# Kernel tuning notes

Hardware: AMD Instinct MI355X
Metric: run time of the kernel (lower is better)

The kernel has to match this reference:

```python
import jax, jax.numpy as jnp
import numpy as np

B, S, D = 4, 2048, 1024
H, DK, DV = 16, 64, 64
TEMP = (4 * DK) ** 0.5
EPS = 1e-6


def setup_inputs() -> dict:
    key = jax.random.key(0)
    ks = jax.random.split(key, 16)
    def lin(k, fin, fout):
        # torch Linear default init: U(-1/sqrt(fin), 1/sqrt(fin)); weight stored [fout,fin], we use [fin,fout]
        bound = 1.0 / np.sqrt(fin)
        return jax.random.uniform(k, (fin, fout), jnp.float32, -bound, bound)
    inp = {}
    for i, name in enumerate(['q_a', 'k_a', 'v_a', 'q_s', 'k_s', 'v_s']):
        inp[name] = jax.random.normal(ks[i], (B, S, D), jnp.float32)
    inp['Wqa'] = lin(ks[6], D, H * DK)
    inp['Wka'] = lin(ks[7], D, H * DK)
    inp['Wva'] = lin(ks[8], D, H * DV)
    inp['Wqs'] = lin(ks[9], D, H * DK)
    inp['Wks'] = lin(ks[10], D, H * DK)
    inp['Wvs'] = lin(ks[11], D, H * DV)
    inp['Wfc'] = lin(ks[12], H * DV, D)
    inp['gamma'] = jnp.ones((D,), jnp.float32)
    inp['beta'] = jnp.zeros((D,), jnp.float32)
    return inp


def _proj(x, W, dh):
    # [B,S,D] @ [D,H*dh] -> [B,H,S,dh]
    b, s, _ = x.shape
    return (x @ W).reshape(b, s, H, dh).transpose(0, 2, 1, 3)


def reference(q_a, k_a, v_a, q_s, k_s, v_s, Wqa, Wka, Wva, Wqs, Wks, Wvs, Wfc, gamma, beta):
    residual = q_a + q_s
    qa = _proj(q_a, Wqa, DK)
    ka = _proj(k_a, Wka, DK)
    va = _proj(v_a, Wva, DV)
    qs = _proj(q_s, Wqs, DK)
    ks = _proj(k_s, Wks, DK)
    vs = _proj(v_s, Wvs, DV)
    # a2a + a2s + s2a + s2s == (qa+qs) @ (ka+ks)^T  (same math, single GEMM)
    scores = jnp.einsum('bhqd,bhkd->bhqk', qa + qs, ka + ks) / TEMP
    attn = jax.nn.softmax(scores, axis=-1)  # [B,H,S,S]
    ctx = jnp.einsum('bhqk,bhkd->bhqd', attn, va + vs)
    ctx = ctx.transpose(0, 2, 1, 3).reshape(q_a.shape[0], q_a.shape[1], H * DV)
    out = ctx @ Wfc + residual
    mu = jnp.mean(out, axis=-1, keepdims=True)
    var = jnp.var(out, axis=-1, keepdims=True)
    out = (out - mu) * jax.lax.rsqrt(var + EPS) * gamma + beta
    return out
```

## Files before the change

### kernel.cpp

```cpp
#include <hip/hip_runtime.h>
#include <hip/hip_bf16.h>
#include <cstdint>
#include <cstddef>

typedef __bf16 bf16;
typedef __bf16 bf16x8 __attribute__((ext_vector_type(8)));
typedef __bf16 bf16x4v __attribute__((ext_vector_type(4)));
typedef __bf16 bf16x2v __attribute__((ext_vector_type(2)));
typedef float f32x4 __attribute__((ext_vector_type(4)));
typedef float f32x16 __attribute__((ext_vector_type(16)));
typedef unsigned uint2v __attribute__((ext_vector_type(2)));
typedef unsigned uint4v __attribute__((ext_vector_type(4)));

#define MFMA16(a, b, c) __builtin_amdgcn_mfma_f32_16x16x32_bf16((a), (b), (c), 0, 0, 0)
#define MFMA32(a, b, c) __builtin_amdgcn_mfma_f32_32x32x16_bf16((a), (b), (c), 0, 0, 0)
#define SWZ(row, byte) ((((row) * 128) + (byte)) ^ (((row) & 7) << 4))

constexpr int BB = 4, SS = 2048, DD = 1024, HH = 16;
constexpr int NROWS = BB * SS;
constexpr size_t NB = (size_t)NROWS * DD;
constexpr size_t NW = (size_t)DD * DD;

static __device__ __forceinline__ unsigned pk2(float a, float b) {
    bf16x2v h;
    h[0] = (bf16)a; h[1] = (bf16)b;
    return __builtin_bit_cast(unsigned, h);
}

static __device__ __forceinline__ bf16x8 frag4(unsigned w0, unsigned w1, unsigned w2, unsigned w3) {
    uint4v u;
    u[0] = w0; u[1] = w1; u[2] = w2; u[3] = w3;
    return __builtin_bit_cast(bf16x8, u);
}

struct Ptrs6 { const float* p[6]; };

__global__ __launch_bounds__(256) void cvt_in_kernel(Ptrs6 src, bf16* dst) {
    const int z = blockIdx.y;
    const size_t idx = (size_t)blockIdx.x * 256 + threadIdx.x;
    float4 v = ((const float4*)src.p[z])[idx];
    bf16x4v o;
    o[0] = (bf16)v.x; o[1] = (bf16)v.y; o[2] = (bf16)v.z; o[3] = (bf16)v.w;
    *(bf16x4v*)(dst + z * NB + idx * 4) = o;
}

struct Ptrs7 { const float* p[7]; };

__global__ __launch_bounds__(256) void cvt_w_kernel(Ptrs7 src, bf16* dst) {
    const int z = blockIdx.z;
    const float* W = src.p[z];
    bf16* WT = dst + (size_t)z * NW;
    __shared__ float tile[32][33];
    const int tx = threadIdx.x, ty = threadIdx.y;
    const int kb = blockIdx.y * 32, nb = blockIdx.x * 32;
#pragma unroll
    for (int j = 0; j < 4; ++j)
        tile[ty + j * 8][tx] = W[(size_t)(kb + ty + j * 8) * DD + nb + tx];
    __syncthreads();
#pragma unroll
    for (int j = 0; j < 4; ++j)
        WT[(size_t)(nb + ty + j * 8) * DD + kb + tx] = (bf16)tile[tx][ty + j * 8];
}

__global__ __launch_bounds__(256) void vt_kernel(const bf16* __restrict__ V,
                                                 bf16* __restrict__ Vt) {
    const int bh = blockIdx.y;
    const int s0 = blockIdx.x * 64;
    __shared__ bf16 t[64][72];
    const int tid = threadIdx.x;
    const int row = tid >> 2, seg = tid & 3;
    const bf16* src = V + ((size_t)bh * SS + s0 + row) * 64 + seg * 16;
    bf16x8 v0 = *(const bf16x8*)src;
    bf16x8 v1 = *(const bf16x8*)(src + 8);
#pragma unroll
    for (int j = 0; j < 8; ++j) {
        t[seg * 16 + j][row] = v0[j];
        t[seg * 16 + 8 + j][row] = v1[j];
    }
    __syncthreads();
    const int d = tid >> 2, c = (tid & 3) * 16;
    bf16x8 o0 = *(const bf16x8*)(&t[d][c]);
    bf16x8 o1 = *(const bf16x8*)(&t[d][c + 8]);
    bf16* dst = Vt + ((size_t)bh * 64 + d) * SS + s0 + c;
    *(bf16x8*)dst = o0;
    *(bf16x8*)(dst + 8) = o1;
}

struct GemmPtrs {
    const bf16* a1[3]; const bf16* a2[3];
    const bf16* b1[3]; const bf16* b2[3];
    bf16* outbh[3];
};

template <int MODE>
__global__ __launch_bounds__(256) void gemm_kernel(GemmPtrs P, int iters, int split,
                                                   float* outF, const float* r1, const float* r2) {
    const int z = blockIdx.z;
    const bf16* __restrict__ A1 = P.a1[z];
    const bf16* __restrict__ A2 = P.a2[z];
    const bf16* __restrict__ B1 = P.b1[z];
    const bf16* __restrict__ B2 = P.b2[z];

    const int tid = threadIdx.x;
    const int lane = tid & 63, w = tid >> 6;
    const int g = lane >> 4, i = lane & 15;
    const int m0 = blockIdx.y * 128, n0 = blockIdx.x * 128;
    const int mb = (w >> 1) * 64, nb = (w & 1) * 64;

    __shared__ __align__(16) bf16 As[128 * 64];
    __shared__ __align__(16) bf16 Bs[128 * 64];

    f32x4 acc[4][4];
#pragma unroll
    for (int a = 0; a < 4; ++a)
#pragma unroll
        for (int b = 0; b < 4; ++b) acc[a][b] = 0.0f;

    for (int kt = 0; kt < iters; ++kt) {
        const bf16* Ag; const bf16* Bg; int koff;
        if (kt < split) { Ag = A1; Bg = B1; koff = kt * 64; }
        else            { Ag = A2; Bg = B2; koff = (kt - split) * 64; }

        __syncthreads();
#pragma unroll
        for (int c = 0; c < 4; ++c) {
            int ci = c * 256 + tid;
            int row = ci >> 3, seg = ci & 7;
            int lb = (row * 128 + seg * 16) ^ ((row & 7) << 4);
            const bf16* ap;
            if (MODE == 0) {
                ap = Ag + (size_t)(m0 + row) * DD + koff + seg * 8;
            } else {
                int gr = m0 + row;
                ap = Ag + ((size_t)((gr >> 11) * HH + (koff >> 6)) * SS + (gr & 2047)) * 64 + seg * 8;
            }
            bf16x8 va = *(const bf16x8*)ap;
            bf16x8 vb = *(const bf16x8*)(Bg + (size_t)(n0 + row) * DD + koff + seg * 8);
            *(bf16x8*)((char*)As + lb) = va;
            *(bf16x8*)((char*)Bs + lb) = vb;
        }
        __syncthreads();

#pragma unroll
        for (int f = 0; f < 2; ++f) {
            bf16x8 af[4], bff[4];
#pragma unroll
            for (int mt = 0; mt < 4; ++mt) {
                int row = mb + mt * 16 + i;
                af[mt] = *(const bf16x8*)((char*)As + ((row * 128 + f * 64 + g * 16) ^ ((row & 7) << 4)));
            }
#pragma unroll
            for (int nt = 0; nt < 4; ++nt) {
                int row = nb + nt * 16 + i;
                bff[nt] = *(const bf16x8*)((char*)Bs + ((row * 128 + f * 64 + g * 16) ^ ((row & 7) << 4)));
            }
#pragma unroll
            for (int mt = 0; mt < 4; ++mt)
#pragma unroll
                for (int nt = 0; nt < 4; ++nt)
                    acc[mt][nt] = MFMA16(af[mt], bff[nt], acc[mt][nt]);
        }
    }

    if (MODE == 0) {
        bf16* outQ = P.outbh[z];
#pragma unroll
        for (int mt = 0; mt < 4; ++mt)
#pragma unroll
            for (int nt = 0; nt < 4; ++nt) {
                int colg = n0 + nb + nt * 16 + i;
                int h = colg >> 6, d = colg & 63;
#pragma unroll
                for (int r = 0; r < 4; ++r) {
                    int rowg = m0 + mb + mt * 16 + g * 4 + r;
                    int b = rowg >> 11, s = rowg & 2047;
                    outQ[(((size_t)(b * HH + h)) * SS + s) * 64 + d] = (bf16)acc[mt][nt][r];
                }
            }
    } else {
#pragma unroll
        for (int mt = 0; mt < 4; ++mt)
#pragma unroll
            for (int nt = 0; nt < 4; ++nt) {
                int colg = n0 + nb + nt * 16 + i;
#pragma unroll
                for (int r = 0; r < 4; ++r) {
                    int rowg = m0 + mb + mt * 16 + g * 4 + r;
                    size_t off = (size_t)rowg * DD + colg;
                    outF[off] = acc[mt][nt][r] + r1[off] + r2[off];
                }
            }
    }
}

__global__ __launch_bounds__(512, 4) void attn_kernel(const bf16* __restrict__ Qg,
                                                      const bf16* __restrict__ Kg,
                                                      const bf16* __restrict__ Vt,
                                                      bf16* __restrict__ ctxh) {
    const int bid = blockIdx.x;
    const int bh = ((bid & 7) << 3) | (bid >> 6);
    const int qt = (bid >> 3) & 7;

    const int tid = threadIdx.x;
    const int lane = tid & 63, w = tid >> 6;
    const int hi = lane >> 5, q = lane & 31;

    __shared__ __align__(16) char smem[32768];

    const int qrow = qt * 256 + w * 32 + q;
    bf16x8 qf[4];
    {
        const bf16* qp = Qg + ((size_t)bh * SS + qrow) * 64;
#pragma unroll
        for (int c = 0; c < 4; ++c) {
            bf16x8 v = *(const bf16x8*)(qp + c * 16 + hi * 8);
#pragma unroll
            for (int e = 0; e < 8; ++e) v[e] = (bf16)((float)v[e] * 0.0625f);
            qf[c] = v;
        }
    }

    const int srow = tid >> 3, sseg = tid & 7;
    const bf16* kgp = Kg + (size_t)bh * SS * 64;
    const bf16* vgp = Vt + (size_t)bh * 64 * SS;
    const int sbyte = SWZ(srow, sseg * 16);

    bf16x8 kreg = *(const bf16x8*)(kgp + (size_t)srow * 64 + sseg * 8);
    bf16x8 vreg = *(const bf16x8*)(vgp + (size_t)srow * SS + sseg * 8);

    f32x16 o0 = {}, o1 = {};
    float m = -3e38f, l = 0.0f;

    for (int kt = 0; kt < SS / 64; ++kt) {
        char* kb_ = smem + (kt & 1) * 16384;
        char* vb_ = kb_ + 8192;
        *(bf16x8*)(kb_ + sbyte) = kreg;
        *(bf16x8*)(vb_ + sbyte) = vreg;
        if (kt + 1 < SS / 64) {
            const int k0n = (kt + 1) * 64;
            kreg = *(const bf16x8*)(kgp + (size_t)(k0n + srow) * 64 + sseg * 8);
            vreg = *(const bf16x8*)(vgp + (size_t)srow * SS + k0n + sseg * 8);
        }
        __syncthreads();

        f32x16 st0 = {}, st1 = {};
#pragma unroll
        for (int c = 0; c < 4; ++c) {
            bf16x8 kf = *(const bf16x8*)(kb_ + SWZ(q, c * 32 + hi * 16));
            st0 = MFMA32(kf, qf[c], st0);
        }
#pragma unroll
        for (int c = 0; c < 4; ++c) {
            bf16x8 kf = *(const bf16x8*)(kb_ + SWZ(32 + q, c * 32 + hi * 16));
            st1 = MFMA32(kf, qf[c], st1);
        }

        float tm = st0[0];
#pragma unroll
        for (int r = 1; r < 16; ++r) tm = fmaxf(tm, st0[r]);
#pragma unroll
        for (int r = 0; r < 16; ++r) tm = fmaxf(tm, st1[r]);
        tm = fmaxf(tm, __shfl_xor(tm, 32, 64));
        if (!__all(tm - m <= 8.0f)) {
            float nm = fmaxf(m, tm);
            float al = __expf(m - nm);
            l *= al;
            o0 *= al;
            o1 *= al;
            m = nm;
        }
        float sum = 0.0f;
#pragma unroll
        for (int r = 0; r < 16; ++r) { st0[r] = __expf(st0[r] - m); sum += st0[r]; }
#pragma unroll
        for (int r = 0; r < 16; ++r) { st1[r] = __expf(st1[r] - m); sum += st1[r]; }
        l += sum;

        bf16x8 pf[4];
#pragma unroll
        for (int c = 0; c < 4; ++c) {
            const f32x16 s_ = (c < 2) ? st0 : st1;
            const int b0 = (c & 1) * 8;
            unsigned a0 = pk2(s_[b0 + 0], s_[b0 + 1]);
            unsigned c0 = pk2(s_[b0 + 4], s_[b0 + 5]);
            unsigned a1 = pk2(s_[b0 + 2], s_[b0 + 3]);
            unsigned c1 = pk2(s_[b0 + 6], s_[b0 + 7]);
            uint2v s1 = __builtin_amdgcn_permlane32_swap(a0, c0, false, false);
            uint2v s2 = __builtin_amdgcn_permlane32_swap(a1, c1, false, false);
            pf[c] = frag4(s1[0], s2[0], s1[1], s2[1]);
        }

#pragma unroll
        for (int c = 0; c < 4; ++c) {
            bf16x8 vf = *(const bf16x8*)(vb_ + SWZ(q, c * 32 + hi * 16));
            o0 = MFMA32(vf, pf[c], o0);
        }
#pragma unroll
        for (int c = 0; c < 4; ++c) {
            bf16x8 vf = *(const bf16x8*)(vb_ + SWZ(32 + q, c * 32 + hi * 16));
            o1 = MFMA32(vf, pf[c], o1);
        }
    }

    float lt = l + __shfl_xor(l, 32, 64);
    float rl = 1.0f / lt;
    __syncthreads();
    const int orow = w * 32 + q;
#pragma unroll
    for (int dh = 0; dh < 2; ++dh) {
#pragma unroll
        for (int r = 0; r < 16; r += 2) {
            float v0 = (dh ? o1[r] : o0[r]) * rl;
            float v1 = (dh ? o1[r + 1] : o0[r + 1]) * rl;
            int d = dh * 32 + (r & 3) + 8 * (r >> 2) + 4 * hi;
            *(unsigned*)(smem + SWZ(orow, d * 2)) = pk2(v0, v1);
        }
    }
    __syncthreads();
    {
        const int row = tid >> 1, hf = tid & 1;
        bf16* outp = ctxh + ((size_t)bh * SS + qt * 256 + row) * 64 + hf * 32;
#pragma unroll
        for (int c = 0; c < 4; ++c) {
            bf16x8 v = *(const bf16x8*)(smem + SWZ(row, hf * 64 + c * 16));
            *(bf16x8*)(outp + c * 8) = v;
        }
    }
}

__global__ __launch_bounds__(256) void ln_kernel(const float* __restrict__ tmp,
                                                 const float* __restrict__ gamma,
                                                 const float* __restrict__ beta,
                                                 float* __restrict__ out) {
    const int row = blockIdx.x;
    const int t = threadIdx.x;
    float4 v = ((const float4*)(tmp + (size_t)row * DD))[t];
    float s = v.x + v.y + v.z + v.w;
    float ss = v.x * v.x + v.y * v.y + v.z * v.z + v.w * v.w;
#pragma unroll
    for (int mask = 1; mask <= 32; mask <<= 1) {
        s += __shfl_xor(s, mask, 64);
        ss += __shfl_xor(ss, mask, 64);
    }
    __shared__ float red[8];
    const int w = t >> 6, lane = t & 63;
    if (lane == 0) { red[w] = s; red[4 + w] = ss; }
    __syncthreads();
    s = red[0] + red[1] + red[2] + red[3];
    ss = red[4] + red[5] + red[6] + red[7];
    const float mu = s * (1.0f / 1024.0f);
    const float var = ss * (1.0f / 1024.0f) - mu * mu;
    const float rs = rsqrtf(var + 1e-6f);
    float4 gm = ((const float4*)gamma)[t];
    float4 bt = ((const float4*)beta)[t];
    float4 ov;
    ov.x = (v.x - mu) * rs * gm.x + bt.x;
    ov.y = (v.y - mu) * rs * gm.y + bt.y;
    ov.z = (v.z - mu) * rs * gm.z + bt.z;
    ov.w = (v.w - mu) * rs * gm.w + bt.w;
    ((float4*)(out + (size_t)row * DD))[t] = ov;
}

extern "C" void kernel_launch(void* const* d_in, const int* in_sizes, int n_in,
                              void* d_out, int out_size, void* d_ws, size_t ws_size,
                              hipStream_t stream) {
    (void)in_sizes; (void)n_in; (void)out_size; (void)ws_size;

    char* ws = (char*)d_ws;
    bf16* xb = (bf16*)ws;
    bf16* wT = (bf16*)(ws + 100663296ull);
    bf16* Qg = (bf16*)(ws + 115343360ull);
    bf16* Kg = (bf16*)(ws + 132120576ull);
    bf16* Vg = (bf16*)(ws + 148897792ull);
    bf16* ctxh = (bf16*)ws;
    bf16* Vtg = (bf16*)(ws + 16777216ull);
    float* tmp = (float*)(ws + 33554432ull);

    {
        Ptrs6 p;
        for (int j = 0; j < 6; ++j) p.p[j] = (const float*)d_in[j];
        cvt_in_kernel<<<dim3(8192, 6), 256, 0, stream>>>(p, xb);
    }
    {
        Ptrs7 p;
        for (int j = 0; j < 7; ++j) p.p[j] = (const float*)d_in[6 + j];
        cvt_w_kernel<<<dim3(32, 32, 7), dim3(32, 8), 0, stream>>>(p, wT);
    }
    {
        GemmPtrs gp;
        gp.a1[0] = xb;           gp.a1[1] = xb + NB;     gp.a1[2] = xb + 2 * NB;
        gp.a2[0] = xb + 3 * NB;  gp.a2[1] = xb + 4 * NB; gp.a2[2] = xb + 5 * NB;
        gp.b1[0] = wT;           gp.b1[1] = wT + NW;     gp.b1[2] = wT + 2 * NW;
        gp.b2[0] = wT + 3 * NW;  gp.b2[1] = wT + 4 * NW; gp.b2[2] = wT + 5 * NW;
        gp.outbh[0] = Qg; gp.outbh[1] = Kg; gp.outbh[2] = Vg;
        gemm_kernel<0><<<dim3(8, 64, 3), 256, 0, stream>>>(gp, 32, 16, nullptr, nullptr, nullptr);
    }
    vt_kernel<<<dim3(32, 64), 256, 0, stream>>>(Vg, Vtg);
    attn_kernel<<<dim3(512), 512, 0, stream>>>(Qg, Kg, Vtg, ctxh);
    {
        GemmPtrs gp;
        for (int j = 0; j < 3; ++j) {
            gp.a1[j] = ctxh; gp.a2[j] = ctxh;
            gp.b1[j] = wT + 6 * NW; gp.b2[j] = wT + 6 * NW;
            gp.outbh[j] = nullptr;
        }
        gemm_kernel<1><<<dim3(8, 64, 1), 256, 0, stream>>>(gp, 16, 16, tmp,
                                                           (const float*)d_in[0],
                                                           (const float*)d_in[3]);
    }
    ln_kernel<<<dim3(8192), 256, 0, stream>>>(tmp, (const float*)d_in[13],
                                              (const float*)d_in[14], (float*)d_out);
}
```

Measured before the change: 552.1 us.

## Use direct global-to-LDS loads, XCD-aware block remap, and MFMA priority hints

```diff
diff --git a/kernel.cpp b/kernel.cpp
--- a/kernel.cpp
+++ b/kernel.cpp
@@ -15,6 +15,9 @@
 #define MFMA16(a, b, c) __builtin_amdgcn_mfma_f32_16x16x32_bf16((a), (b), (c), 0, 0, 0)
 #define MFMA32(a, b, c) __builtin_amdgcn_mfma_f32_32x32x16_bf16((a), (b), (c), 0, 0, 0)
 #define SWZ(row, byte) ((((row) * 128) + (byte)) ^ (((row) & 7) << 4))
+#define GLOAD_LDS(g, l) \
+    __builtin_amdgcn_global_load_lds((const __attribute__((address_space(1))) void*)(g), \
+                                     (__attribute__((address_space(3))) void*)(l), 16, 0, 0)
 
 constexpr int BB = 4, SS = 2048, DD = 1024, HH = 16;
 constexpr int NROWS = BB * SS;
@@ -95,7 +98,13 @@
 template <int MODE>
 __global__ __launch_bounds__(256) void gemm_kernel(GemmPtrs P, int iters, int split,
                                                    float* outF, const float* r1, const float* r2) {
-    const int z = blockIdx.z;
+    const int cpx = gridDim.x >> 3;
+    const int bid0 = blockIdx.x;
+    const int work = (bid0 & 7) * cpx + (bid0 >> 3);
+    const int z = work >> 9;
+    const int rem = work & 511;
+    const int m0 = (rem >> 3) * 128, n0 = (rem & 7) * 128;
+
     const bf16* __restrict__ A1 = P.a1[z];
     const bf16* __restrict__ A2 = P.a2[z];
     const bf16* __restrict__ B1 = P.b1[z];
@@ -104,17 +113,19 @@
     const int tid = threadIdx.x;
     const int lane = tid & 63, w = tid >> 6;
     const int g = lane >> 4, i = lane & 15;
-    const int m0 = blockIdx.y * 128, n0 = blockIdx.x * 128;
     const int mb = (w >> 1) * 64, nb = (w & 1) * 64;
 
     __shared__ __align__(16) bf16 As[128 * 64];
     __shared__ __align__(16) bf16 Bs[128 * 64];
 
+    const int lrow = lane >> 3, lseg = lane & 7;
+    const int chunk = lseg ^ lrow;
+
     f32x4 acc[4][4];
 #pragma unroll
-    for (int a = 0; a < 4; ++a)
-#pragma unroll
-        for (int b = 0; b < 4; ++b) acc[a][b] = 0.0f;
+    for (int aa = 0; aa < 4; ++aa)
+#pragma unroll
+        for (int bb = 0; bb < 4; ++bb) acc[aa][bb] = 0.0f;
 
     for (int kt = 0; kt < iters; ++kt) {
         const bf16* Ag; const bf16* Bg; int koff;
@@ -124,20 +135,17 @@
         __syncthreads();
 #pragma unroll
         for (int c = 0; c < 4; ++c) {
-            int ci = c * 256 + tid;
-            int row = ci >> 3, seg = ci & 7;
-            int lb = (row * 128 + seg * 16) ^ ((row & 7) << 4);
+            const int row = (w * 4 + c) * 8 + lrow;
             const bf16* ap;
             if (MODE == 0) {
-                ap = Ag + (size_t)(m0 + row) * DD + koff + seg * 8;
+                ap = Ag + (size_t)(m0 + row) * DD + koff + chunk * 8;
             } else {
                 int gr = m0 + row;
-                ap = Ag + ((size_t)((gr >> 11) * HH + (koff >> 6)) * SS + (gr & 2047)) * 64 + seg * 8;
+                ap = Ag + ((size_t)((gr >> 11) * HH + (koff >> 6)) * SS + (gr & 2047)) * 64 + chunk * 8;
             }
-            bf16x8 va = *(const bf16x8*)ap;
-            bf16x8 vb = *(const bf16x8*)(Bg + (size_t)(n0 + row) * DD + koff + seg * 8);
-            *(bf16x8*)((char*)As + lb) = va;
-            *(bf16x8*)((char*)Bs + lb) = vb;
+            const bf16* bp = Bg + (size_t)(n0 + row) * DD + koff + chunk * 8;
+            GLOAD_LDS(ap, As + (w * 4 + c) * 512);
+            GLOAD_LDS(bp, Bs + (w * 4 + c) * 512);
         }
         __syncthreads();
 
@@ -147,12 +155,12 @@
 #pragma unroll
             for (int mt = 0; mt < 4; ++mt) {
                 int row = mb + mt * 16 + i;
-                af[mt] = *(const bf16x8*)((char*)As + ((row * 128 + f * 64 + g * 16) ^ ((row & 7) << 4)));
+                af[mt] = *(const bf16x8*)((char*)As + SWZ(row, f * 64 + g * 16));
             }
 #pragma unroll
             for (int nt = 0; nt < 4; ++nt) {
                 int row = nb + nt * 16 + i;
-                bff[nt] = *(const bf16x8*)((char*)Bs + ((row * 128 + f * 64 + g * 16) ^ ((row & 7) << 4)));
+                bff[nt] = *(const bf16x8*)((char*)Bs + SWZ(row, f * 64 + g * 16));
             }
 #pragma unroll
             for (int mt = 0; mt < 4; ++mt)
@@ -244,6 +252,7 @@
         __syncthreads();
 
         f32x16 st0 = {}, st1 = {};
+        __builtin_amdgcn_s_setprio(1);
 #pragma unroll
         for (int c = 0; c < 4; ++c) {
             bf16x8 kf = *(const bf16x8*)(kb_ + SWZ(q, c * 32 + hi * 16));
@@ -254,6 +263,7 @@
             bf16x8 kf = *(const bf16x8*)(kb_ + SWZ(32 + q, c * 32 + hi * 16));
             st1 = MFMA32(kf, qf[c], st1);
         }
+        __builtin_amdgcn_s_setprio(0);
 
         float tm = st0[0];
 #pragma unroll
@@ -290,6 +300,7 @@
             pf[c] = frag4(s1[0], s2[0], s1[1], s2[1]);
         }
 
+        __builtin_amdgcn_s_setprio(1);
 #pragma unroll
         for (int c = 0; c < 4; ++c) {
             bf16x8 vf = *(const bf16x8*)(vb_ + SWZ(q, c * 32 + hi * 16));
@@ -300,6 +311,7 @@
             bf16x8 vf = *(const bf16x8*)(vb_ + SWZ(32 + q, c * 32 + hi * 16));
             o1 = MFMA32(vf, pf[c], o1);
         }
+        __builtin_amdgcn_s_setprio(0);
     }
 
     float lt = l + __shfl_xor(l, 32, 64);
@@ -393,7 +405,7 @@
         gp.b1[0] = wT;           gp.b1[1] = wT + NW;     gp.b1[2] = wT + 2 * NW;
         gp.b2[0] = wT + 3 * NW;  gp.b2[1] = wT + 4 * NW; gp.b2[2] = wT + 5 * NW;
         gp.outbh[0] = Qg; gp.outbh[1] = Kg; gp.outbh[2] = Vg;
-        gemm_kernel<0><<<dim3(8, 64, 3), 256, 0, stream>>>(gp, 32, 16, nullptr, nullptr, nullptr);
+        gemm_kernel<0><<<dim3(1536), 256, 0, stream>>>(gp, 32, 16, nullptr, nullptr, nullptr);
     }
     vt_kernel<<<dim3(32, 64), 256, 0, stream>>>(Vg, Vtg);
     attn_kernel<<<dim3(512), 512, 0, stream>>>(Qg, Kg, Vtg, ctxh);
@@ -404,9 +416,9 @@
             gp.b1[j] = wT + 6 * NW; gp.b2[j] = wT + 6 * NW;
             gp.outbh[j] = nullptr;
         }
-        gemm_kernel<1><<<dim3(8, 64, 1), 256, 0, stream>>>(gp, 16, 16, tmp,
-                                                           (const float*)d_in[0],
-                                                           (const float*)d_in[3]);
+        gemm_kernel<1><<<dim3(512), 256, 0, stream>>>(gp, 16, 16, tmp,
+                                                      (const float*)d_in[0],
+                                                      (const float*)d_in[3]);
     }
     ln_kernel<<<dim3(8192), 256, 0, stream>>>(tmp, (const float*)d_in[13],
                                               (const float*)d_in[14], (float*)d_out);
```

New measurement: 533.0 us. 3.5% less time.
